# Kernel optimization log

Measured on AMD Instinct MI355X. Metric: run time of the kernel, lower is better.

## Reference

```python
import jax, jax.numpy as jnp
import numpy as np

BSZ, L, H, P = 8, 4096, 512, 256  # batch, seq len, features, complex state dim (conj_sym)
DT_MIN, DT_MAX = 1e-3, 1e-1


def setup_inputs() -> dict:
    key = jax.random.key(0)
    k_u, k_B, k_C, k_D, k_dt = jax.random.split(key, 5)
    u = jax.random.normal(k_u, (BSZ, L, H), dtype=jnp.float32)
    # HiPPO-like stable init for the diagonal state matrix
    Lambda_re = -0.5 * jnp.ones((P,), dtype=jnp.float32)
    Lambda_im = jnp.pi * jnp.arange(P, dtype=jnp.float32)
    # lecun-normal-ish scaling for real/imag parts of B (fan_in = H) and C (fan_in = P)
    B = jax.random.normal(k_B, (P, H, 2), dtype=jnp.float32) / jnp.sqrt(2.0 * H)
    C = jax.random.normal(k_C, (H, P, 2), dtype=jnp.float32) / jnp.sqrt(2.0 * P)
    D = jax.random.normal(k_D, (H,), dtype=jnp.float32)
    log_step = jax.random.uniform(k_dt, (P, 1), dtype=jnp.float32,
                                  minval=jnp.log(DT_MIN), maxval=jnp.log(DT_MAX))
    return {"u": u, "Lambda_re": Lambda_re, "Lambda_im": Lambda_im,
            "B": B, "C": C, "D": D, "log_step": log_step}


def _binop(q_i, q_j):
    """Associative binary operator for diagonal linear recurrence."""
    A_i, b_i = q_i
    A_j, b_j = q_j
    return (A_j * A_i, A_j * b_i + b_j)


def reference(u, Lambda_re, Lambda_im, B, C, D, log_step):
    # --- setup / discretization (zero-order hold) ---
    Lambda = (Lambda_re + 1j * Lambda_im).astype(jnp.complex64)      # (P,)
    B_tilde = (B[..., 0] + 1j * B[..., 1]).astype(jnp.complex64)     # (P,H)
    C_tilde = (C[..., 0] + 1j * C[..., 1]).astype(jnp.complex64)     # (H,P)
    step = jnp.exp(log_step[:, 0])                                   # (P,)
    Lambda_bar = jnp.exp(Lambda * step)                              # (P,)
    B_bar = ((Lambda_bar - 1.0) / Lambda)[:, None] * B_tilde         # (P,H)

    # --- parallel scan over the sequence (diagonal SSM) ---
    Bu = jnp.einsum('blh,ph->blp', u, B_bar)                         # (B,L,P) complex64
    Lam = jnp.broadcast_to(Lambda_bar, Bu.shape)                     # (B,L,P)
    _, xs = jax.lax.associative_scan(_binop, (Lam, Bu), axis=1)      # (B,L,P)

    # --- emissions (factor 2 from conjugate symmetry) + feedthrough ---
    ys = 2.0 * jnp.einsum('blp,hp->blh', xs, C_tilde).real + D * u   # (B,L,H)
    return jax.nn.gelu(ys)
```

## Files before the change

kernel.cpp:

```cpp
#include <hip/hip_runtime.h>
#include <cstdint>
#include <cstddef>

typedef unsigned short u16;
typedef short short8 __attribute__((ext_vector_type(8)));
typedef float floatx4 __attribute__((ext_vector_type(4)));

#define DEVINL __device__ __forceinline__

static constexpr int BSZ = 8, SEQL = 4096, H = 512, P = 256;
static constexpr int M = BSZ * SEQL;
static constexpr int KD = 512;
static constexpr int ND = 512;
static constexpr int CHUNK = 64;
static constexpr int NCH = SEQL / CHUNK;

DEVINL u16 f2bf(float f) {
  union { float f; unsigned u; } v; v.f = f;
  unsigned r = (v.u + 0x7fffu + ((v.u >> 16) & 1u)) >> 16;
  return (u16)r;
}
DEVINL float bf2f(u16 h) {
  union { unsigned u; float f; } v; v.u = ((unsigned)h) << 16; return v.f;
}

DEVINL void gload_lds16(const void* g, void* l) {
  __builtin_amdgcn_global_load_lds(
      (const __attribute__((address_space(1))) unsigned*)g,
      (__attribute__((address_space(3))) unsigned*)l, 16, 0, 0);
}

DEVINL float2 lam_of(int p, const float* __restrict__ Lre, const float* __restrict__ Lim,
                     const float* __restrict__ lstep) {
  float lr = Lre[p], li = Lim[p];
  float st = expf(lstep[p]);
  float mag = expf(lr * st);
  float ang = li * st;
  return make_float2(mag * cosf(ang), mag * sinf(ang));
}

__global__ void prep_kernel(const float2* __restrict__ Bin, const float* __restrict__ Cin,
                            const float* __restrict__ Lre, const float* __restrict__ Lim,
                            const float* __restrict__ lstep,
                            u16* __restrict__ bt1, u16* __restrict__ bt2) {
  int bid = blockIdx.x;
  if (bid < 512) {
    int idx = bid * 256 + threadIdx.x;
    int p = idx / H, h = idx % H;
    float lr = Lre[p], li = Lim[p];
    float st = expf(lstep[p]);
    float mag = expf(lr * st);
    float ang = li * st;
    float cr = mag * cosf(ang), ci = mag * sinf(ang);
    float a = cr - 1.0f, b = ci;
    float den = lr * lr + li * li;
    float fr = (a * lr + b * li) / den;
    float fi = (b * lr - a * li) / den;
    float2 bv = Bin[(size_t)p * H + h];
    float br = fr * bv.x - fi * bv.y;
    float bi = fr * bv.y + fi * bv.x;
    bt1[(size_t)(2 * p) * H + h]     = f2bf(br);
    bt1[(size_t)(2 * p + 1) * H + h] = f2bf(bi);
  } else {
    int idx = (bid - 512) * 256 + threadIdx.x;
    float c = Cin[idx];
    float v = (idx & 1) ? -2.0f * c : 2.0f * c;
    bt2[idx] = f2bf(v);
  }
}

__global__ __launch_bounds__(256, 3) void gemm0(const float* __restrict__ Af32,
                                                const u16* __restrict__ Bt,
                                                u16* __restrict__ outBf) {
  __shared__ float Asf[2][128 * 32];
  __shared__ u16   Bs[2][128 * 32];
  const int tid = threadIdx.x;
  const int bm = blockIdx.x, bn = blockIdx.y;
  const int wave = tid >> 6, lane = tid & 63;
  const int quad = lane >> 4, l16 = lane & 15;
  const int wm = (wave & 1) << 6, wn = (wave >> 1) << 6;

  floatx4 acc[4][4] = {};

  const float* Ab = Af32 + (size_t)bm * 128 * KD;
  const u16*   Bb = Bt + (size_t)bn * 128 * KD;
  const int srowA = tid >> 3;
  const int scolA = (((tid & 7) ^ ((tid >> 3) & 7)) << 2);
  const int srowB = tid >> 2;
  const int scolB = (tid & 3) << 3;

#define STAGE0(buf, kofs)                                                                     \
  do {                                                                                        \
    gload_lds16(Ab + (size_t)srowA * KD + (kofs) + scolA,        &Asf[buf][tid * 4]);         \
    gload_lds16(Ab + (size_t)(srowA + 32) * KD + (kofs) + scolA, &Asf[buf][1024 + tid * 4]);  \
    gload_lds16(Ab + (size_t)(srowA + 64) * KD + (kofs) + scolA, &Asf[buf][2048 + tid * 4]);  \
    gload_lds16(Ab + (size_t)(srowA + 96) * KD + (kofs) + scolA, &Asf[buf][3072 + tid * 4]);  \
    gload_lds16(Bb + (size_t)srowB * KD + (kofs) + scolB,        &Bs[buf][tid * 8]);          \
    gload_lds16(Bb + (size_t)(srowB + 64) * KD + (kofs) + scolB, &Bs[buf][2048 + tid * 8]);   \
  } while (0)

  STAGE0(0, 0);
  asm volatile("s_waitcnt vmcnt(0)" ::: "memory");
  __builtin_amdgcn_sched_barrier(0);
  __builtin_amdgcn_s_barrier();

  const int c0 = ((quad << 1) ^ (l16 & 7));
  const int c1 = c0 ^ 1;

  int cur = 0;
  for (int k0 = 0; k0 < KD; k0 += 32) {
    if (k0 + 32 < KD) STAGE0(cur ^ 1, k0 + 32);

    short8 af[4], bfr[4];
#pragma unroll
    for (int t = 0; t < 4; t++) {
      const float* rowp = &Asf[cur][(wm + t * 16 + l16) * 32];
      float4 a0 = *(const float4*)(rowp + c0 * 4);
      float4 a1 = *(const float4*)(rowp + c1 * 4);
      af[t][0] = (short)f2bf(a0.x); af[t][1] = (short)f2bf(a0.y);
      af[t][2] = (short)f2bf(a0.z); af[t][3] = (short)f2bf(a0.w);
      af[t][4] = (short)f2bf(a1.x); af[t][5] = (short)f2bf(a1.y);
      af[t][6] = (short)f2bf(a1.z); af[t][7] = (short)f2bf(a1.w);
    }
#pragma unroll
    for (int t = 0; t < 4; t++)
      bfr[t] = *(const short8*)&Bs[cur][(wn + t * 16 + l16) * 32 + quad * 8];

    asm volatile("s_waitcnt lgkmcnt(0)" ::: "memory");
    __builtin_amdgcn_sched_barrier(0);

    __builtin_amdgcn_s_setprio(1);
#pragma unroll
    for (int tm = 0; tm < 4; tm++)
#pragma unroll
      for (int tn = 0; tn < 4; tn++)
        acc[tm][tn] = __builtin_amdgcn_mfma_f32_16x16x32_bf16(af[tm], bfr[tn], acc[tm][tn], 0, 0, 0);
    __builtin_amdgcn_s_setprio(0);

    asm volatile("s_waitcnt vmcnt(0)" ::: "memory");
    __builtin_amdgcn_sched_barrier(0);
    __builtin_amdgcn_s_barrier();
    cur ^= 1;
  }
#undef STAGE0

  const int row_base = bm * 128 + wm + quad * 4;
  const int col_base = bn * 128 + wn + l16;
#pragma unroll
  for (int tm = 0; tm < 4; tm++)
#pragma unroll
    for (int tn = 0; tn < 4; tn++) {
      int n = col_base + tn * 16;
#pragma unroll
      for (int r = 0; r < 4; r++) {
        int m = row_base + tm * 16 + r;
        outBf[(size_t)m * ND + n] = f2bf(acc[tm][tn][r]);
      }
    }
}

__global__ __launch_bounds__(256, 4) void gemm1(const u16* __restrict__ A,
                                                const u16* __restrict__ Bt,
                                                float* __restrict__ outF,
                                                const float* __restrict__ Dv,
                                                const float* __restrict__ U32) {
  __shared__ u16 As[2][128 * 32];
  __shared__ u16 Bs[2][128 * 32];
  const int tid = threadIdx.x;
  const int bm = blockIdx.x, bn = blockIdx.y;
  const int wave = tid >> 6, lane = tid & 63;
  const int quad = lane >> 4, l16 = lane & 15;
  const int wm = (wave & 1) << 6, wn = (wave >> 1) << 6;

  floatx4 acc[4][4] = {};

  const u16* Ab = A + (size_t)bm * 128 * KD;
  const u16* Bb = Bt + (size_t)bn * 128 * KD;
  const int srow = tid >> 2;
  const int scol = (tid & 3) << 3;

#define STAGE1(buf, kofs)                                                                  \
  do {                                                                                     \
    gload_lds16(Ab + (size_t)srow * KD + (kofs) + scol,        &As[buf][tid * 8]);         \
    gload_lds16(Ab + (size_t)(srow + 64) * KD + (kofs) + scol, &As[buf][2048 + tid * 8]);  \
    gload_lds16(Bb + (size_t)srow * KD + (kofs) + scol,        &Bs[buf][tid * 8]);         \
    gload_lds16(Bb + (size_t)(srow + 64) * KD + (kofs) + scol, &Bs[buf][2048 + tid * 8]);  \
  } while (0)

  STAGE1(0, 0);
  asm volatile("s_waitcnt vmcnt(0)" ::: "memory");
  __builtin_amdgcn_sched_barrier(0);
  __builtin_amdgcn_s_barrier();

  int cur = 0;
  for (int k0 = 0; k0 < KD; k0 += 32) {
    if (k0 + 32 < KD) STAGE1(cur ^ 1, k0 + 32);

    short8 af[4], bfr[4];
#pragma unroll
    for (int t = 0; t < 4; t++)
      af[t] = *(const short8*)&As[cur][(wm + t * 16 + l16) * 32 + quad * 8];
#pragma unroll
    for (int t = 0; t < 4; t++)
      bfr[t] = *(const short8*)&Bs[cur][(wn + t * 16 + l16) * 32 + quad * 8];

    asm volatile("s_waitcnt lgkmcnt(0)" ::: "memory");
    __builtin_amdgcn_sched_barrier(0);

    __builtin_amdgcn_s_setprio(1);
#pragma unroll
    for (int tm = 0; tm < 4; tm++)
#pragma unroll
      for (int tn = 0; tn < 4; tn++)
        acc[tm][tn] = __builtin_amdgcn_mfma_f32_16x16x32_bf16(af[tm], bfr[tn], acc[tm][tn], 0, 0, 0);
    __builtin_amdgcn_s_setprio(0);

    asm volatile("s_waitcnt vmcnt(0)" ::: "memory");
    __builtin_amdgcn_sched_barrier(0);
    __builtin_amdgcn_s_barrier();
    cur ^= 1;
  }
#undef STAGE1

  const int row_base = bm * 128 + wm + quad * 4;
  const int col_base = bn * 128 + wn + l16;
  float dv[4];
#pragma unroll
  for (int tn = 0; tn < 4; tn++) dv[tn] = Dv[col_base + tn * 16];
#pragma unroll
  for (int tm = 0; tm < 4; tm++)
#pragma unroll
    for (int tn = 0; tn < 4; tn++) {
      int n = col_base + tn * 16;
#pragma unroll
      for (int r = 0; r < 4; r++) {
        int m = row_base + tm * 16 + r;
        float ys = acc[tm][tn][r] + dv[tn] * U32[(size_t)m * ND + n];
        float zz = ys + 0.044715f * (ys * ys * ys);
        float e = __builtin_amdgcn_exp2f(-2.3022082f * zz);
        outF[(size_t)m * ND + n] = ys * __builtin_amdgcn_rcpf(1.0f + e);
      }
    }
}

__global__ __launch_bounds__(256) void scan_carry(const u16* __restrict__ Bu,
                                                  const float* __restrict__ Lre,
                                                  const float* __restrict__ Lim,
                                                  const float* __restrict__ lstep,
                                                  float2* __restrict__ carry) {
  int p = threadIdx.x;
  int c = blockIdx.x;
  int b = blockIdx.y;
  float2 lm = lam_of(p, Lre, Lim, lstep);
  float xr = 0.f, xi = 0.f;
  const u16* base = Bu + ((size_t)b * SEQL + (size_t)c * CHUNK) * 512 + 2 * p;
  for (int l = 0; l < CHUNK; l++) {
    unsigned w = *(const unsigned*)(base + (size_t)l * 512);
    float br = bf2f((u16)(w & 0xffffu));
    float bi = bf2f((u16)(w >> 16));
    float nr = lm.x * xr - lm.y * xi + br;
    float ni = lm.x * xi + lm.y * xr + bi;
    xr = nr; xi = ni;
  }
  carry[((size_t)b * NCH + c) * P + p] = make_float2(xr, xi);
}

__global__ __launch_bounds__(256) void scan_apply(u16* __restrict__ Bu,
                                                  const float* __restrict__ Lre,
                                                  const float* __restrict__ Lim,
                                                  const float* __restrict__ lstep,
                                                  const float2* __restrict__ carry) {
  int p = threadIdx.x;
  int c = blockIdx.x;
  int b = blockIdx.y;
  float2 lm = lam_of(p, Lre, Lim, lstep);
  float ar = lm.x, ai = lm.y;
  for (int i = 0; i < 6; i++) { float nr = ar * ar - ai * ai, ni = 2.f * ar * ai; ar = nr; ai = ni; }
  float pr = 0.f, pi = 0.f;
  const float2* cb_base = carry + (size_t)b * NCH * P + p;
  for (int j0 = 0; j0 < c; j0 += 16) {
    float2 cb[16];
#pragma unroll
    for (int t = 0; t < 16; t++) {
      int j = j0 + t;
      int jc = j < c ? j : c - 1;
      cb[t] = cb_base[(size_t)jc * P];
    }
#pragma unroll
    for (int t = 0; t < 16; t++) {
      bool real = (j0 + t) < c;
      float mr = real ? ar : 1.0f;
      float mi = real ? ai : 0.0f;
      float cx = real ? cb[t].x : 0.0f;
      float cy = real ? cb[t].y : 0.0f;
      float nr = mr * pr - mi * pi + cx;
      float ni = mr * pi + mi * pr + cy;
      pr = nr; pi = ni;
    }
  }
  float xr = pr, xi = pi;
  u16* base = Bu + ((size_t)b * SEQL + (size_t)c * CHUNK) * 512 + 2 * p;
  for (int l = 0; l < CHUNK; l++) {
    unsigned* addr = (unsigned*)(base + (size_t)l * 512);
    unsigned w = *addr;
    float br = bf2f((u16)(w & 0xffffu));
    float bi = bf2f((u16)(w >> 16));
    float nr = lm.x * xr - lm.y * xi + br;
    float ni = lm.x * xi + lm.y * xr + bi;
    xr = nr; xi = ni;
    *addr = (unsigned)f2bf(nr) | ((unsigned)f2bf(ni) << 16);
  }
}

extern "C" void kernel_launch(void* const* d_in, const int* in_sizes, int n_in,
                              void* d_out, int out_size, void* d_ws, size_t ws_size,
                              hipStream_t stream) {
  const float* u      = (const float*)d_in[0];
  const float* Lre    = (const float*)d_in[1];
  const float* Lim    = (const float*)d_in[2];
  const float* Bin    = (const float*)d_in[3];
  const float* Cin    = (const float*)d_in[4];
  const float* Dv     = (const float*)d_in[5];
  const float* lstep  = (const float*)d_in[6];
  float* out          = (float*)d_out;

  char* ws = (char*)d_ws;
  u16*    bt1    = (u16*)   (ws + 0);
  u16*    bt2    = (u16*)   (ws + 524288);
  u16*    Bu     = (u16*)   (ws + 1048576);
  float2* carry  = (float2*)(ws + 34603008);

  prep_kernel<<<1536, 256, 0, stream>>>((const float2*)Bin, Cin, Lre, Lim, lstep, bt1, bt2);

  gemm0<<<dim3(M / 128, ND / 128), 256, 0, stream>>>(u, bt1, Bu);

  scan_carry<<<dim3(NCH, BSZ), 256, 0, stream>>>(Bu, Lre, Lim, lstep, carry);
  scan_apply<<<dim3(NCH, BSZ), 256, 0, stream>>>(Bu, Lre, Lim, lstep, carry);

  gemm1<<<dim3(M / 128, ND / 128), 256, 0, stream>>>(Bu, bt2, out, Dv, u);
}
```

Baseline: 208.5 us.

## Fuse chunk carry computation into input GEMM epilogue and double scan chunk size

Removes the separate scan_carry kernel. Each gemm0 tile now computes the chunk-end state for its 128 rows and 64 complex state columns, reading back its own freshly written bf16 output through global memory (likely still in L2). The chunk length rises to 128 to match the GEMM tile, which halves the number of chunks but doubles the serial work per scan_apply thread. The scan loops are also batched into groups of 8 loads to expose memory-level parallelism. The cost is a serial 128-step tail in only one wave per GEMM block, which lengthens each block.

```diff
diff --git a/kernel.cpp b/kernel.cpp
--- a/kernel.cpp
+++ b/kernel.cpp
@@ -12,7 +12,7 @@
 static constexpr int M = BSZ * SEQL;
 static constexpr int KD = 512;
 static constexpr int ND = 512;
-static constexpr int CHUNK = 64;
+static constexpr int CHUNK = 128;
 static constexpr int NCH = SEQL / CHUNK;
 
 DEVINL u16 f2bf(float f) {
@@ -71,7 +71,11 @@
 
 __global__ __launch_bounds__(256, 3) void gemm0(const float* __restrict__ Af32,
                                                 const u16* __restrict__ Bt,
-                                                u16* __restrict__ outBf) {
+                                                u16* __restrict__ outBf,
+                                                const float* __restrict__ Lre,
+                                                const float* __restrict__ Lim,
+                                                const float* __restrict__ lstep,
+                                                float2* __restrict__ carry) {
   __shared__ float Asf[2][128 * 32];
   __shared__ u16   Bs[2][128 * 32];
   const int tid = threadIdx.x;
@@ -157,6 +161,31 @@
         outBf[(size_t)m * ND + n] = f2bf(acc[tm][tn][r]);
       }
     }
+
+  __syncthreads();
+  if (tid < 64) {
+    const int lp = tid;
+    const int p = bn * 64 + lp;
+    const int cix = bm & 31, b = bm >> 5;
+    float2 lm = lam_of(p, Lre, Lim, lstep);
+    const u16* tb = outBf + (size_t)(bm * 128) * ND + bn * 128 + 2 * lp;
+    float xr = 0.f, xi = 0.f;
+    for (int l0 = 0; l0 < 128; l0 += 8) {
+      unsigned w[8];
+#pragma unroll
+      for (int t = 0; t < 8; t++)
+        w[t] = *(const unsigned*)(tb + (size_t)(l0 + t) * ND);
+#pragma unroll
+      for (int t = 0; t < 8; t++) {
+        float br = bf2f((u16)(w[t] & 0xffffu));
+        float bi = bf2f((u16)(w[t] >> 16));
+        float nr = lm.x * xr - lm.y * xi + br;
+        float ni = lm.x * xi + lm.y * xr + bi;
+        xr = nr; xi = ni;
+      }
+    }
+    carry[((size_t)b * NCH + cix) * P + p] = make_float2(xr, xi);
+  }
 }
 
 __global__ __launch_bounds__(256, 4) void gemm1(const u16* __restrict__ A,
@@ -243,28 +272,6 @@
     }
 }
 
-__global__ __launch_bounds__(256) void scan_carry(const u16* __restrict__ Bu,
-                                                  const float* __restrict__ Lre,
-                                                  const float* __restrict__ Lim,
-                                                  const float* __restrict__ lstep,
-                                                  float2* __restrict__ carry) {
-  int p = threadIdx.x;
-  int c = blockIdx.x;
-  int b = blockIdx.y;
-  float2 lm = lam_of(p, Lre, Lim, lstep);
-  float xr = 0.f, xi = 0.f;
-  const u16* base = Bu + ((size_t)b * SEQL + (size_t)c * CHUNK) * 512 + 2 * p;
-  for (int l = 0; l < CHUNK; l++) {
-    unsigned w = *(const unsigned*)(base + (size_t)l * 512);
-    float br = bf2f((u16)(w & 0xffffu));
-    float bi = bf2f((u16)(w >> 16));
-    float nr = lm.x * xr - lm.y * xi + br;
-    float ni = lm.x * xi + lm.y * xr + bi;
-    xr = nr; xi = ni;
-  }
-  carry[((size_t)b * NCH + c) * P + p] = make_float2(xr, xi);
-}
-
 __global__ __launch_bounds__(256) void scan_apply(u16* __restrict__ Bu,
                                                   const float* __restrict__ Lre,
                                                   const float* __restrict__ Lim,
@@ -275,7 +282,8 @@
   int b = blockIdx.y;
   float2 lm = lam_of(p, Lre, Lim, lstep);
   float ar = lm.x, ai = lm.y;
-  for (int i = 0; i < 6; i++) { float nr = ar * ar - ai * ai, ni = 2.f * ar * ai; ar = nr; ai = ni; }
+#pragma unroll
+  for (int i = 0; i < 7; i++) { float nr = ar * ar - ai * ai, ni = 2.f * ar * ai; ar = nr; ai = ni; }
   float pr = 0.f, pi = 0.f;
   const float2* cb_base = carry + (size_t)b * NCH * P + p;
   for (int j0 = 0; j0 < c; j0 += 16) {
@@ -300,15 +308,20 @@
   }
   float xr = pr, xi = pi;
   u16* base = Bu + ((size_t)b * SEQL + (size_t)c * CHUNK) * 512 + 2 * p;
-  for (int l = 0; l < CHUNK; l++) {
-    unsigned* addr = (unsigned*)(base + (size_t)l * 512);
-    unsigned w = *addr;
-    float br = bf2f((u16)(w & 0xffffu));
-    float bi = bf2f((u16)(w >> 16));
-    float nr = lm.x * xr - lm.y * xi + br;
-    float ni = lm.x * xi + lm.y * xr + bi;
-    xr = nr; xi = ni;
-    *addr = (unsigned)f2bf(nr) | ((unsigned)f2bf(ni) << 16);
+  for (int l0 = 0; l0 < CHUNK; l0 += 8) {
+    unsigned w[8];
+#pragma unroll
+    for (int t = 0; t < 8; t++)
+      w[t] = *(const unsigned*)(base + (size_t)(l0 + t) * 512);
+#pragma unroll
+    for (int t = 0; t < 8; t++) {
+      float br = bf2f((u16)(w[t] & 0xffffu));
+      float bi = bf2f((u16)(w[t] >> 16));
+      float nr = lm.x * xr - lm.y * xi + br;
+      float ni = lm.x * xi + lm.y * xr + bi;
+      xr = nr; xi = ni;
+      *(unsigned*)(base + (size_t)(l0 + t) * 512) = (unsigned)f2bf(nr) | ((unsigned)f2bf(ni) << 16);
+    }
   }
 }
 
@@ -332,9 +345,8 @@
 
   prep_kernel<<<1536, 256, 0, stream>>>((const float2*)Bin, Cin, Lre, Lim, lstep, bt1, bt2);
 
-  gemm0<<<dim3(M / 128, ND / 128), 256, 0, stream>>>(u, bt1, Bu);
-
-  scan_carry<<<dim3(NCH, BSZ), 256, 0, stream>>>(Bu, Lre, Lim, lstep, carry);
+  gemm0<<<dim3(M / 128, ND / 128), 256, 0, stream>>>(u, bt1, Bu, Lre, Lim, lstep, carry);
+
   scan_apply<<<dim3(NCH, BSZ), 256, 0, stream>>>(Bu, Lre, Lim, lstep, carry);
 
   gemm1<<<dim3(M / 128, ND / 128), 256, 0, stream>>>(Bu, bt2, out, Dv, u);
```

After: 221.3 us. 6.2% more time.
